# Kernel tuning notes

Measured on AMD Instinct MI355X. Metric: run time of the kernel, lower is better.

The kernel has to match this reference:

```python
import jax, jax.numpy as jnp
import numpy as np

N = 100000      # nodes
E = 1600000     # edges
F_IN = 256      # input features
HID = 64        # hidden channels
C = 10          # classes
EPS = 0.3       # FAGCN epsilon (raw-feature residual scale)
NUM_LAYERS = 2


def setup_inputs() -> dict:
    key = jax.random.key(0)
    ks = jax.random.split(key, 8)
    x = jax.random.normal(ks[0], (N, F_IN), dtype=jnp.float32)
    edge_index = jax.random.randint(ks[1], (2, E), 0, N, dtype=jnp.int32)
    # lin1 / lin2 (xavier-normal-ish scale)
    w1 = jax.random.normal(ks[2], (HID, F_IN), dtype=jnp.float32) * (1.414 / np.sqrt(F_IN))
    b1 = jnp.zeros((HID,), dtype=jnp.float32)
    w2 = jax.random.normal(ks[3], (C, HID), dtype=jnp.float32) * (1.414 / np.sqrt(HID))
    b2 = jnp.zeros((C,), dtype=jnp.float32)
    # per-layer FAConv attention vectors att_l, att_r: [NUM_LAYERS, HID]
    att_l = jax.random.normal(ks[4], (NUM_LAYERS, HID), dtype=jnp.float32) * (1.0 / np.sqrt(HID))
    att_r = jax.random.normal(ks[5], (NUM_LAYERS, HID), dtype=jnp.float32) * (1.0 / np.sqrt(HID))
    return {"x": x, "edge_index": edge_index, "w1": w1, "b1": b1,
            "w2": w2, "b2": b2, "att_l": att_l, "att_r": att_r}


def reference(x, edge_index, w1, b1, w2, b2, att_l, att_r):
    src = edge_index[0]  # [E] message source j
    dst = edge_index[1]  # [E] aggregation target i

    # gcn_norm without self-loops: deg from destination, symmetric normalization
    deg = jax.ops.segment_sum(jnp.ones((E,), x.dtype), dst, num_segments=N)
    dis = jnp.where(deg > 0, jax.lax.rsqrt(jnp.maximum(deg, 1.0)), 0.0)
    norm = dis[src] * dis[dst]  # [E]

    h = jax.nn.relu(x @ w1.T + b1)  # [N, HID]
    raw = h
    for l in range(NUM_LAYERS):
        al = h @ att_l[l]  # [N] per-node left score
        ar = h @ att_r[l]  # [N] per-node right score
        # alpha_j (att_l at source) + alpha_i (att_r at destination)
        alpha = jnp.tanh(al[src] + ar[dst])  # [E]
        msg = h[src] * (alpha * norm)[:, None]  # [E, HID]
        agg = jax.ops.segment_sum(msg, dst, num_segments=N)  # [N, HID]
        h = agg + EPS * raw

    logits = h @ w2.T + b2  # [N, C]
    return jax.nn.log_softmax(logits, axis=1)
```

## Files before the change

kernel.cpp:

```cpp
#include <hip/hip_runtime.h>

#define NN 100000
#define NE 1600000
#define FIN 256
#define HID 64
#define NCLS 10
#define EPSF 0.3f


__global__ void k_wt(const float* __restrict__ w1, float* __restrict__ w1T) {
    int t = blockIdx.x * 256 + threadIdx.x;
    if (t < HID * FIN) {
        int k = t >> 6;
        int h = t & 63;
        w1T[t] = w1[h * FIN + k];
    }
}

__global__ void k_deg(const int* __restrict__ ei, int* __restrict__ deg) {
    int e = blockIdx.x * 256 + threadIdx.x;
    if (e < NE) atomicAdd(&deg[ei[NE + e]], 1);
}

__global__ void k_dis(const int* __restrict__ deg, float* __restrict__ dis) {
    int i = blockIdx.x * 256 + threadIdx.x;
    if (i < NN) {
        int d = deg[i];
        dis[i] = (d > 0) ? (1.0f / sqrtf((float)d)) : 0.0f;
    }
}

__global__ void k_scan1(const int* __restrict__ deg, int* __restrict__ rp, int* __restrict__ bsum) {
    __shared__ int s[1024];
    int i = blockIdx.x * 1024 + threadIdx.x;
    int v = (i < NN) ? deg[i] : 0;
    s[threadIdx.x] = v;
    __syncthreads();
    for (int off = 1; off < 1024; off <<= 1) {
        int t = (threadIdx.x >= off) ? s[threadIdx.x - off] : 0;
        __syncthreads();
        s[threadIdx.x] += t;
        __syncthreads();
    }
    if (i < NN) rp[i] = s[threadIdx.x] - v;
    if (threadIdx.x == 1023) bsum[blockIdx.x] = s[1023];
}

__global__ void k_scan2(int* __restrict__ bsum, int nb) {
    __shared__ int s[128];
    int v = (threadIdx.x < nb) ? bsum[threadIdx.x] : 0;
    s[threadIdx.x] = v;
    __syncthreads();
    for (int off = 1; off < 128; off <<= 1) {
        int t = (threadIdx.x >= off) ? s[threadIdx.x - off] : 0;
        __syncthreads();
        s[threadIdx.x] += t;
        __syncthreads();
    }
    if (threadIdx.x < nb) bsum[threadIdx.x] = s[threadIdx.x] - v;
}

__global__ void k_scan3(int* __restrict__ rp, const int* __restrict__ bsum) {
    int i = blockIdx.x * 1024 + threadIdx.x;
    if (i < NN) rp[i] += bsum[blockIdx.x];
    if (i == 0) rp[NN] = NE;
}

__global__ void k_fill(const int* __restrict__ ei, const int* __restrict__ rp,
                       int* __restrict__ cursor, int2* __restrict__ csr) {
    int e = blockIdx.x * 256 + threadIdx.x;
    if (e < NE) {
        int s = ei[e], d = ei[NE + e];
        int pos = rp[d] + atomicAdd(&cursor[d], 1);
        csr[pos] = make_int2(s, d);
    }
}


__global__ __launch_bounds__(64) void k_gemm1(const float* __restrict__ x, const float* __restrict__ w1T,
                                              const float* __restrict__ b1, const float* __restrict__ dis,
                                              const float* __restrict__ att_l0, const float* __restrict__ att_r0,
                                              float* __restrict__ h,
                                              float2* __restrict__ aldis, float2* __restrict__ ardis) {
    int n = blockIdx.x * 64 + threadIdx.x;
    if (n >= NN) return;
    float acc[HID];
#pragma unroll
    for (int j = 0; j < HID; j++) acc[j] = b1[j];
    const float4* __restrict__ xr = reinterpret_cast<const float4*>(x + (size_t)n * FIN);
    const float4* __restrict__ wr = reinterpret_cast<const float4*>(w1T);
    for (int k4 = 0; k4 < FIN / 4; k4++) {
        float4 xv = xr[k4];
        const float* xf = &xv.x;
#pragma unroll
        for (int kk = 0; kk < 4; kk++) {
            float xs = xf[kk];
            const float4* wrow = wr + (size_t)(k4 * 4 + kk) * (HID / 4);
#pragma unroll
            for (int hq = 0; hq < HID / 4; hq++) {
                float4 wq = wrow[hq];
                acc[hq * 4 + 0] = fmaf(xs, wq.x, acc[hq * 4 + 0]);
                acc[hq * 4 + 1] = fmaf(xs, wq.y, acc[hq * 4 + 1]);
                acc[hq * 4 + 2] = fmaf(xs, wq.z, acc[hq * 4 + 2]);
                acc[hq * 4 + 3] = fmaf(xs, wq.w, acc[hq * 4 + 3]);
            }
        }
    }
    float4* __restrict__ ho = reinterpret_cast<float4*>(h + (size_t)n * HID);
    float p = 0.0f, q = 0.0f;
#pragma unroll
    for (int hq = 0; hq < HID / 4; hq++) {
        float4 v;
        v.x = fmaxf(acc[hq * 4 + 0], 0.0f);
        v.y = fmaxf(acc[hq * 4 + 1], 0.0f);
        v.z = fmaxf(acc[hq * 4 + 2], 0.0f);
        v.w = fmaxf(acc[hq * 4 + 3], 0.0f);
        ho[hq] = v;
        p = fmaf(v.x, att_l0[hq * 4 + 0], p); q = fmaf(v.x, att_r0[hq * 4 + 0], q);
        p = fmaf(v.y, att_l0[hq * 4 + 1], p); q = fmaf(v.y, att_r0[hq * 4 + 1], q);
        p = fmaf(v.z, att_l0[hq * 4 + 2], p); q = fmaf(v.z, att_r0[hq * 4 + 2], q);
        p = fmaf(v.w, att_l0[hq * 4 + 3], p); q = fmaf(v.w, att_r0[hq * 4 + 3], q);
    }
    float ds = dis[n];
    aldis[n] = make_float2(p, ds);
    ardis[n] = make_float2(q, ds);
}

__global__ void k_coef(const int2* __restrict__ csr, const float2* __restrict__ aldis,
                       const float2* __restrict__ ardis, float* __restrict__ coef) {
    int e = blockIdx.x * 256 + threadIdx.x;
    if (e < NE) {
        int2 sd = csr[e];
        float2 al = aldis[sd.x];
        float2 ar = ardis[sd.y];
        coef[e] = tanhf(al.x + ar.x) * (al.y * ar.y);
    }
}

template <int MODE>
__global__ __launch_bounds__(256) void k_agg(const float* __restrict__ h_in, const float* __restrict__ raw,
                                             const int* __restrict__ rp, const int2* __restrict__ csr,
                                             const float* __restrict__ coef, float* __restrict__ h_out,
                                             const float* __restrict__ att_l, const float* __restrict__ att_r,
                                             const float* __restrict__ dis,
                                             float2* __restrict__ aldis, float2* __restrict__ ardis,
                                             const float* __restrict__ w2, const float* __restrict__ b2,
                                             float* __restrict__ out) {
    int lane = threadIdx.x & 63;
    int i = blockIdx.x * 4 + (threadIdx.x >> 6);
    if (i >= NN) return;
    float acc = EPSF * raw[(size_t)i * HID + lane];
    int e0 = rp[i], e1 = rp[i + 1];
    int deg = e1 - e0;
    float a0 = 0.0f, a1 = 0.0f, a2 = 0.0f, a3 = 0.0f;
    for (int base = 0; base < deg; base += 64) {
        int rem = deg - base; if (rem > 64) rem = 64;
        int j = 0; float c = 0.0f;
        if (lane < rem) {
            j = csr[e0 + base + lane].x;
            c = coef[e0 + base + lane];
        }
        int t = 0;
        for (; t + 4 <= rem; t += 4) {
            int j0 = __shfl(j, t, 64), j1 = __shfl(j, t + 1, 64);
            int j2 = __shfl(j, t + 2, 64), j3 = __shfl(j, t + 3, 64);
            float c0 = __shfl(c, t, 64), c1 = __shfl(c, t + 1, 64);
            float c2 = __shfl(c, t + 2, 64), c3 = __shfl(c, t + 3, 64);
            float h0 = h_in[(size_t)j0 * HID + lane];
            float h1 = h_in[(size_t)j1 * HID + lane];
            float h2 = h_in[(size_t)j2 * HID + lane];
            float h3 = h_in[(size_t)j3 * HID + lane];
            a0 = fmaf(h0, c0, a0);
            a1 = fmaf(h1, c1, a1);
            a2 = fmaf(h2, c2, a2);
            a3 = fmaf(h3, c3, a3);
        }
        for (; t < rem; ++t) {
            int jj = __shfl(j, t, 64);
            float cc = __shfl(c, t, 64);
            a0 = fmaf(h_in[(size_t)jj * HID + lane], cc, a0);
        }
    }
    acc += (a0 + a1) + (a2 + a3);

    if (MODE == 2) {
        float lg[NCLS];
#pragma unroll
        for (int cc = 0; cc < NCLS; cc++) {
            float p = acc * w2[cc * HID + lane];
#pragma unroll
            for (int m = 1; m < 64; m <<= 1) p += __shfl_xor(p, m, 64);
            lg[cc] = p + b2[cc];
        }
        float mx = lg[0];
#pragma unroll
        for (int cc = 1; cc < NCLS; cc++) mx = fmaxf(mx, lg[cc]);
        float ssum = 0.0f;
#pragma unroll
        for (int cc = 0; cc < NCLS; cc++) ssum += expf(lg[cc] - mx);
        float r = mx + logf(ssum);
        if (lane < NCLS) {
            float v = 0.0f;
#pragma unroll
            for (int cc = 0; cc < NCLS; cc++)
                if (lane == cc) v = lg[cc];
            out[(size_t)i * NCLS + lane] = v - r;
        }
    } else {
        h_out[(size_t)i * HID + lane] = acc;
        if (MODE == 1) {
            float p = acc * att_l[lane];
            float q = acc * att_r[lane];
#pragma unroll
            for (int m = 1; m < 64; m <<= 1) {
                p += __shfl_xor(p, m, 64);
                q += __shfl_xor(q, m, 64);
            }
            if (lane == 0) {
                float ds = dis[i];
                aldis[i] = make_float2(p, ds);
                ardis[i] = make_float2(q, ds);
            }
        }
    }
}


extern "C" void kernel_launch(void* const* d_in, const int* in_sizes, int n_in,
                              void* d_out, int out_size, void* d_ws, size_t ws_size,
                              hipStream_t stream) {
    const float* x     = (const float*)d_in[0];
    const int*   ei    = (const int*)d_in[1];
    const float* w1    = (const float*)d_in[2];
    const float* b1    = (const float*)d_in[3];
    const float* w2    = (const float*)d_in[4];
    const float* b2    = (const float*)d_in[5];
    const float* att_l = (const float*)d_in[6];
    const float* att_r = (const float*)d_in[7];
    float* out = (float*)d_out;

    char* ws = (char*)d_ws;
    size_t off = 0;
    auto take = [&](size_t bytes) -> void* {
        void* p = ws + off;
        off += (bytes + 255) & ~(size_t)255;
        return p;
    };
    int*    deg     = (int*)take((size_t)NN * 4);
    int*    cursor  = (int*)take((size_t)NN * 4);
    int*    rp      = (int*)take((size_t)(NN + 1) * 4);
    int*    bsum    = (int*)take(128 * 4);
    float*  dis     = (float*)take((size_t)NN * 4);
    float2* aldis   = (float2*)take((size_t)NN * 8);
    float2* ardis   = (float2*)take((size_t)NN * 8);
    float*  w1T     = (float*)take((size_t)HID * FIN * 4);
    int2*   csr     = (int2*)take((size_t)NE * 8);
    float*  coef    = (float*)take((size_t)NE * 4);
    float*  hA      = (float*)take((size_t)NN * HID * 4);
    float*  hB      = (float*)take((size_t)NN * HID * 4);

    hipMemsetAsync(deg, 0, (size_t)NN * 4, stream);
    hipMemsetAsync(cursor, 0, (size_t)NN * 4, stream);

    const int EB = (NE + 255) / 256;
    const int NB = (NN + 255) / 256;
    const int SB = (NN + 1023) / 1024;

    k_wt<<<64, 256, 0, stream>>>(w1, w1T);
    k_deg<<<EB, 256, 0, stream>>>(ei, deg);
    k_dis<<<NB, 256, 0, stream>>>(deg, dis);
    k_scan1<<<SB, 1024, 0, stream>>>(deg, rp, bsum);
    k_scan2<<<1, 128, 0, stream>>>(bsum, SB);
    k_scan3<<<SB, 1024, 0, stream>>>(rp, bsum);
    k_fill<<<EB, 256, 0, stream>>>(ei, rp, cursor, csr);

    k_gemm1<<<(NN + 63) / 64, 64, 0, stream>>>(x, w1T, b1, dis, att_l, att_r, hA, aldis, ardis);

    k_coef<<<EB, 256, 0, stream>>>(csr, aldis, ardis, coef);
    k_agg<1><<<NN / 4, 256, 0, stream>>>(hA, hA, rp, csr, coef, hB,
                                         att_l + HID, att_r + HID, dis, aldis, ardis,
                                         nullptr, nullptr, nullptr);

    k_coef<<<EB, 256, 0, stream>>>(csr, aldis, ardis, coef);
    k_agg<2><<<NN / 4, 256, 0, stream>>>(hB, hA, rp, csr, coef, nullptr,
                                         nullptr, nullptr, nullptr, nullptr, nullptr,
                                         w2, b2, out);
}
```

Measured before the change: 594.0 us.

## Fuse edge coefficient into aggregation, shrink CSR, stage W1 in LDS

Drops the separate k_coef kernel and computes each edge's tanh attention times norm coefficient inside the aggregation wave, gathering the source node's score and reading the destination's once per row. The CSR stores only source indices, which halves CSR bytes and removes the coef array round trip. Score buffers are double-buffered so layer 1 can write the next layer's scores while reading the current ones. The first GEMM now uses 256-thread blocks, loads W1 into shared memory, and prefetches the next x vector. The trade-off is more tanh work and score gathers inside the latency-bound aggregation loop, plus a 64 KB LDS footprint per GEMM block.

```diff
diff --git a/kernel.cpp b/kernel.cpp
--- a/kernel.cpp
+++ b/kernel.cpp
@@ -67,35 +67,44 @@
 }
 
 __global__ void k_fill(const int* __restrict__ ei, const int* __restrict__ rp,
-                       int* __restrict__ cursor, int2* __restrict__ csr) {
+                       int* __restrict__ cursor, int* __restrict__ csr_src) {
     int e = blockIdx.x * 256 + threadIdx.x;
     if (e < NE) {
         int s = ei[e], d = ei[NE + e];
         int pos = rp[d] + atomicAdd(&cursor[d], 1);
-        csr[pos] = make_int2(s, d);
-    }
-}
-
-
-__global__ __launch_bounds__(64) void k_gemm1(const float* __restrict__ x, const float* __restrict__ w1T,
-                                              const float* __restrict__ b1, const float* __restrict__ dis,
-                                              const float* __restrict__ att_l0, const float* __restrict__ att_r0,
-                                              float* __restrict__ h,
-                                              float2* __restrict__ aldis, float2* __restrict__ ardis) {
-    int n = blockIdx.x * 64 + threadIdx.x;
-    if (n >= NN) return;
+        csr_src[pos] = s;
+    }
+}
+
+
+__global__ __launch_bounds__(256) void k_gemm1(const float* __restrict__ x, const float* __restrict__ w1T,
+                                               const float* __restrict__ b1, const float* __restrict__ dis,
+                                               const float* __restrict__ att_l0, const float* __restrict__ att_r0,
+                                               float* __restrict__ h,
+                                               float2* __restrict__ aldis, float2* __restrict__ ardis) {
+    __shared__ float4 wlds[FIN * (HID / 4)];
+    const float4* __restrict__ wr = reinterpret_cast<const float4*>(w1T);
+    for (int t = threadIdx.x; t < FIN * (HID / 4); t += 256) wlds[t] = wr[t];
+    __syncthreads();
+
+    int n = blockIdx.x * 256 + threadIdx.x;
+    bool act = (n < NN);
+    int nc = act ? n : (NN - 1);
     float acc[HID];
 #pragma unroll
     for (int j = 0; j < HID; j++) acc[j] = b1[j];
-    const float4* __restrict__ xr = reinterpret_cast<const float4*>(x + (size_t)n * FIN);
-    const float4* __restrict__ wr = reinterpret_cast<const float4*>(w1T);
+    const float4* __restrict__ xr = reinterpret_cast<const float4*>(x + (size_t)nc * FIN);
+
+    float4 cur = xr[0];
+#pragma unroll 1
     for (int k4 = 0; k4 < FIN / 4; k4++) {
-        float4 xv = xr[k4];
-        const float* xf = &xv.x;
+        float4 nxt = make_float4(0.f, 0.f, 0.f, 0.f);
+        if (k4 < FIN / 4 - 1) nxt = xr[k4 + 1];
+        const float* xf = &cur.x;
 #pragma unroll
         for (int kk = 0; kk < 4; kk++) {
             float xs = xf[kk];
-            const float4* wrow = wr + (size_t)(k4 * 4 + kk) * (HID / 4);
+            const float4* wrow = &wlds[(k4 * 4 + kk) * (HID / 4)];
 #pragma unroll
             for (int hq = 0; hq < HID / 4; hq++) {
                 float4 wq = wrow[hq];
@@ -105,7 +114,10 @@
                 acc[hq * 4 + 3] = fmaf(xs, wq.w, acc[hq * 4 + 3]);
             }
         }
-    }
+        cur = nxt;
+    }
+
+    if (!act) return;
     float4* __restrict__ ho = reinterpret_cast<float4*>(h + (size_t)n * HID);
     float p = 0.0f, q = 0.0f;
 #pragma unroll
@@ -126,46 +138,38 @@
     ardis[n] = make_float2(q, ds);
 }
 
-__global__ void k_coef(const int2* __restrict__ csr, const float2* __restrict__ aldis,
-                       const float2* __restrict__ ardis, float* __restrict__ coef) {
-    int e = blockIdx.x * 256 + threadIdx.x;
-    if (e < NE) {
-        int2 sd = csr[e];
-        float2 al = aldis[sd.x];
-        float2 ar = ardis[sd.y];
-        coef[e] = tanhf(al.x + ar.x) * (al.y * ar.y);
-    }
-}
-
 template <int MODE>
 __global__ __launch_bounds__(256) void k_agg(const float* __restrict__ h_in, const float* __restrict__ raw,
-                                             const int* __restrict__ rp, const int2* __restrict__ csr,
-                                             const float* __restrict__ coef, float* __restrict__ h_out,
+                                             const int* __restrict__ rp, const int* __restrict__ csr_src,
+                                             const float2* __restrict__ aldis_i, const float2* __restrict__ ardis_i,
+                                             float* __restrict__ h_out,
                                              const float* __restrict__ att_l, const float* __restrict__ att_r,
                                              const float* __restrict__ dis,
-                                             float2* __restrict__ aldis, float2* __restrict__ ardis,
+                                             float2* __restrict__ aldis_o, float2* __restrict__ ardis_o,
                                              const float* __restrict__ w2, const float* __restrict__ b2,
                                              float* __restrict__ out) {
     int lane = threadIdx.x & 63;
     int i = blockIdx.x * 4 + (threadIdx.x >> 6);
     if (i >= NN) return;
+    float2 ai = ardis_i[i];
     float acc = EPSF * raw[(size_t)i * HID + lane];
     int e0 = rp[i], e1 = rp[i + 1];
     int deg = e1 - e0;
     float a0 = 0.0f, a1 = 0.0f, a2 = 0.0f, a3 = 0.0f;
     for (int base = 0; base < deg; base += 64) {
         int rem = deg - base; if (rem > 64) rem = 64;
-        int j = 0; float c = 0.0f;
+        int j = 0; float cf = 0.0f;
         if (lane < rem) {
-            j = csr[e0 + base + lane].x;
-            c = coef[e0 + base + lane];
+            j = csr_src[e0 + base + lane];
+            float2 aj = aldis_i[j];
+            cf = tanhf(aj.x + ai.x) * (aj.y * ai.y);
         }
         int t = 0;
         for (; t + 4 <= rem; t += 4) {
             int j0 = __shfl(j, t, 64), j1 = __shfl(j, t + 1, 64);
             int j2 = __shfl(j, t + 2, 64), j3 = __shfl(j, t + 3, 64);
-            float c0 = __shfl(c, t, 64), c1 = __shfl(c, t + 1, 64);
-            float c2 = __shfl(c, t + 2, 64), c3 = __shfl(c, t + 3, 64);
+            float c0 = __shfl(cf, t, 64), c1 = __shfl(cf, t + 1, 64);
+            float c2 = __shfl(cf, t + 2, 64), c3 = __shfl(cf, t + 3, 64);
             float h0 = h_in[(size_t)j0 * HID + lane];
             float h1 = h_in[(size_t)j1 * HID + lane];
             float h2 = h_in[(size_t)j2 * HID + lane];
@@ -177,7 +181,7 @@
         }
         for (; t < rem; ++t) {
             int jj = __shfl(j, t, 64);
-            float cc = __shfl(c, t, 64);
+            float cc = __shfl(cf, t, 64);
             a0 = fmaf(h_in[(size_t)jj * HID + lane], cc, a0);
         }
     }
@@ -218,8 +222,8 @@
             }
             if (lane == 0) {
                 float ds = dis[i];
-                aldis[i] = make_float2(p, ds);
-                ardis[i] = make_float2(q, ds);
+                aldis_o[i] = make_float2(p, ds);
+                ardis_o[i] = make_float2(q, ds);
             }
         }
     }
@@ -251,11 +255,12 @@
     int*    rp      = (int*)take((size_t)(NN + 1) * 4);
     int*    bsum    = (int*)take(128 * 4);
     float*  dis     = (float*)take((size_t)NN * 4);
-    float2* aldis   = (float2*)take((size_t)NN * 8);
-    float2* ardis   = (float2*)take((size_t)NN * 8);
+    float2* aldisA  = (float2*)take((size_t)NN * 8);
+    float2* ardisA  = (float2*)take((size_t)NN * 8);
+    float2* aldisB  = (float2*)take((size_t)NN * 8);
+    float2* ardisB  = (float2*)take((size_t)NN * 8);
     float*  w1T     = (float*)take((size_t)HID * FIN * 4);
-    int2*   csr     = (int2*)take((size_t)NE * 8);
-    float*  coef    = (float*)take((size_t)NE * 4);
+    int*    csr_src = (int*)take((size_t)NE * 4);
     float*  hA      = (float*)take((size_t)NN * HID * 4);
     float*  hB      = (float*)take((size_t)NN * HID * 4);
 
@@ -272,17 +277,15 @@
     k_scan1<<<SB, 1024, 0, stream>>>(deg, rp, bsum);
     k_scan2<<<1, 128, 0, stream>>>(bsum, SB);
     k_scan3<<<SB, 1024, 0, stream>>>(rp, bsum);
-    k_fill<<<EB, 256, 0, stream>>>(ei, rp, cursor, csr);
-
-    k_gemm1<<<(NN + 63) / 64, 64, 0, stream>>>(x, w1T, b1, dis, att_l, att_r, hA, aldis, ardis);
-
-    k_coef<<<EB, 256, 0, stream>>>(csr, aldis, ardis, coef);
-    k_agg<1><<<NN / 4, 256, 0, stream>>>(hA, hA, rp, csr, coef, hB,
-                                         att_l + HID, att_r + HID, dis, aldis, ardis,
+    k_fill<<<EB, 256, 0, stream>>>(ei, rp, cursor, csr_src);
+
+    k_gemm1<<<(NN + 255) / 256, 256, 0, stream>>>(x, w1T, b1, dis, att_l, att_r, hA, aldisA, ardisA);
+
+    k_agg<1><<<NN / 4, 256, 0, stream>>>(hA, hA, rp, csr_src, aldisA, ardisA, hB,
+                                         att_l + HID, att_r + HID, dis, aldisB, ardisB,
                                          nullptr, nullptr, nullptr);
 
-    k_coef<<<EB, 256, 0, stream>>>(csr, aldis, ardis, coef);
-    k_agg<2><<<NN / 4, 256, 0, stream>>>(hB, hA, rp, csr, coef, nullptr,
+    k_agg<2><<<NN / 4, 256, 0, stream>>>(hB, hA, rp, csr_src, aldisB, ardisB, nullptr,
                                          nullptr, nullptr, nullptr, nullptr, nullptr,
                                          w2, b2, out);
 }
```

New measurement: 557.0 us. 6.2% less time.
